# Performance work log

Measured on AMD Instinct MI355X. Metric: run time of the kernel, lower is better.

Reference implementation:

```python
import jax, jax.numpy as jnp
import numpy as np

B, N, C = 4, 2048, 768
H = 12
DH = C // H
HID = int(C * 4.0)
SCALE = DH ** -0.5
EPS = 1e-5


def layernorm(x, g, b):
    mu = jnp.mean(x, axis=-1, keepdims=True)
    var = jnp.var(x, axis=-1, keepdims=True)
    return (x - mu) * jax.lax.rsqrt(var + EPS) * g + b


def setup_inputs() -> dict:
    key = jax.random.key(0)
    ks = jax.random.split(key, 10)
    s = lambda fan_in: 1.0 / np.sqrt(fan_in)
    return {
        "x": jax.random.normal(ks[0], (B, N, C), dtype=jnp.float32),
        "ln1_g": jnp.ones((C,), jnp.float32),
        "ln1_b": jnp.zeros((C,), jnp.float32),
        "w_qkv": jax.random.uniform(ks[1], (C, 3 * C), jnp.float32, -s(C), s(C)),
        "w_proj": jax.random.uniform(ks[2], (C, C), jnp.float32, -s(C), s(C)),
        "b_proj": jnp.zeros((C,), jnp.float32),
        "ln2_g": jnp.ones((C,), jnp.float32),
        "ln2_b": jnp.zeros((C,), jnp.float32),
        "w_fc1": jax.random.uniform(ks[3], (C, HID), jnp.float32, -s(C), s(C)),
        "b_fc1": jnp.zeros((HID,), jnp.float32),
        "w_fc2": jax.random.uniform(ks[4], (HID, C), jnp.float32, -s(HID), s(HID)),
        "b_fc2": jnp.zeros((C,), jnp.float32),
    }


def reference(x, ln1_g, ln1_b, w_qkv, w_proj, b_proj, ln2_g, ln2_b, w_fc1, b_fc1, w_fc2, b_fc2):
    # --- attention branch ---
    h = layernorm(x, ln1_g, ln1_b)                       # [B,N,C]
    qkv = (h @ w_qkv).reshape(B, N, 3, H, DH)
    q = qkv[:, :, 0].transpose(0, 2, 1, 3)               # [B,H,N,DH]
    k = qkv[:, :, 1].transpose(0, 2, 1, 3)
    v = qkv[:, :, 2].transpose(0, 2, 1, 3)
    attn = jnp.einsum('bhnd,bhmd->bhnm', q, k) * SCALE   # [B,H,N,N]
    attn = jax.nn.softmax(attn, axis=-1)
    y = jnp.einsum('bhnm,bhmd->bhnd', attn, v)           # [B,H,N,DH]
    y = y.transpose(0, 2, 1, 3).reshape(B, N, C)
    y = y @ w_proj + b_proj
    x = x + y
    # --- MLP branch ---
    h = layernorm(x, ln2_g, ln2_b)
    h = jax.nn.gelu(h @ w_fc1 + b_fc1, approximate=False)
    h = h @ w_fc2 + b_fc2
    return x + h
```

## Files before the change

kernel.cpp:

```cpp
#include <hip/hip_runtime.h>
#include <stdint.h>

#define DEV __device__ __forceinline__

typedef __attribute__((ext_vector_type(8))) short bf16x8;
typedef __attribute__((ext_vector_type(4))) float f32x4;
typedef __attribute__((ext_vector_type(4))) short s16x4;

DEV short f2bf(float f) {
    union { float f; unsigned u; } v; v.f = f;
    unsigned r = v.u + 0x7fffu + ((v.u >> 16) & 1u);
    return (short)(r >> 16);
}

DEV uint32_t cvtpk(float lo, float hi) {
    uint32_t r;
    asm("v_cvt_pk_bf16_f32 %0, %1, %2" : "=v"(r) : "v"(lo), "v"(hi));
    return r;
}

typedef const unsigned int __attribute__((address_space(1)))* gp1;
typedef unsigned int __attribute__((address_space(3)))* lp3;

DEV void gload16(const void* g, void* l) {
    __builtin_amdgcn_global_load_lds((gp1)g, (lp3)l, 16, 0, 0);
}

DEV void wait4_barrier() { asm volatile("s_waitcnt vmcnt(4)\ns_barrier" ::: "memory"); }
DEV void wait2_barrier() { asm volatile("s_waitcnt vmcnt(2)\ns_barrier" ::: "memory"); }
DEV void wait0_barrier() { asm volatile("s_waitcnt vmcnt(0)\ns_barrier" ::: "memory"); }

__global__ __launch_bounds__(256) void tcvt(
    const float* __restrict__ W, short* __restrict__ WT, int K, int N)
{
    __shared__ float t[32][33];
    int n0 = blockIdx.x * 32, k0 = blockIdx.y * 32;
    int tx = threadIdx.x & 31, ty = threadIdx.x >> 5;
#pragma unroll
    for (int i = 0; i < 32; i += 8)
        t[ty + i][tx] = W[(size_t)(k0 + ty + i) * N + n0 + tx];
    __syncthreads();
#pragma unroll
    for (int i = 0; i < 32; i += 8)
        WT[(size_t)(n0 + ty + i) * K + k0 + tx] = f2bf(t[tx][ty + i]);
}

__global__ __launch_bounds__(256) void ln_bf16(
    const float* __restrict__ x, const float* __restrict__ gam,
    const float* __restrict__ bet, short* __restrict__ out)
{
    const int w = threadIdx.x >> 6, lane = threadIdx.x & 63;
    const size_t row = (size_t)blockIdx.x * 4 + w;
    const float* xr = x + row * 768;
    float4 v[3];
    float s = 0.f, ss = 0.f;
#pragma unroll
    for (int k = 0; k < 3; ++k) {
        v[k] = *(const float4*)(xr + k * 256 + lane * 4);
        s  += v[k].x + v[k].y + v[k].z + v[k].w;
        ss += v[k].x * v[k].x + v[k].y * v[k].y + v[k].z * v[k].z + v[k].w * v[k].w;
    }
#pragma unroll
    for (int i = 1; i < 64; i <<= 1) { s += __shfl_xor(s, i, 64); ss += __shfl_xor(ss, i, 64); }
    const float inv = 1.f / 768.f;
    float mu = s * inv;
    float var = ss * inv - mu * mu;
    float rstd = rsqrtf(var + 1e-5f);
#pragma unroll
    for (int k = 0; k < 3; ++k) {
        int c = k * 256 + lane * 4;
        float vv[4] = { v[k].x, v[k].y, v[k].z, v[k].w };
        s16x4 o;
#pragma unroll
        for (int j = 0; j < 4; ++j)
            o[j] = f2bf((vv[j] - mu) * rstd * gam[c + j] + bet[c + j]);
        *(s16x4*)(out + row * 768 + c) = o;
    }
}

template<int MODE>
DEV void gemm_body(
    const short* __restrict__ A, const short* __restrict__ Bt,
    int M, int N, int K,
    const float* __restrict__ bias, const float* __restrict__ resid,
    float* __restrict__ outf, short* __restrict__ outb,
    short* __restrict__ qo, short* __restrict__ ko, short* __restrict__ vo,
    char* lds)
{
    const int tid = threadIdx.x;
    const int w = tid >> 6, lane = tid & 63;
    const int g = lane >> 4, l15 = lane & 15;
    const int brow = blockIdx.x * 128, bcol = blockIdx.y * 128;
    const int wr = w >> 2, wc = w & 3;
    f32x4 acc[4][2] = {};

    int aoff[4], boff[2];
#pragma unroll
    for (int m = 0; m < 4; ++m) {
        int ra = wr * 64 + m * 16 + l15;
        aoff[m] = ra * 64 + ((g * 16) ^ (((ra >> 1) & 3) << 4));
    }
#pragma unroll
    for (int n = 0; n < 2; ++n) {
        int rb = wc * 32 + n * 16 + l15;
        boff[n] = 8192 + rb * 64 + ((g * 16) ^ (((rb >> 1) & 3) << 4));
    }
    const int dStage = tid * 16;
    const char* pA; const char* pB;
    {
        int r = dStage >> 6, b = dStage & 63;
        int bs = b ^ (((r >> 1) & 3) << 4);
        pA = (const char*)(A  + (size_t)(brow + r) * K) + bs;
        pB = (const char*)(Bt + (size_t)(bcol + r) * K) + bs;
    }

#define GSTAGE(BUF, OFF) do { \
    gload16(pA + (OFF), lds + (BUF) * 16384 + dStage); \
    gload16(pB + (OFF), lds + (BUF) * 16384 + 8192 + dStage); } while (0)

    const int KT = K >> 5;
    GSTAGE(0, 0);
    GSTAGE(1, 64);
    wait2_barrier();

    const int NM = KT / 3;
    for (int mi = 0; mi < NM; ++mi) {
#pragma unroll
        for (int u = 0; u < 3; ++u) {
            const int s = mi * 3 + u;
            if (s + 2 < KT) GSTAGE((u + 2) % 3, (u + 2) * 64);
            bf16x8 af[4], bfg[2];
#pragma unroll
            for (int m = 0; m < 4; ++m)
                af[m]  = *(const bf16x8*)(lds + u * 16384 + aoff[m]);
#pragma unroll
            for (int n = 0; n < 2; ++n)
                bfg[n] = *(const bf16x8*)(lds + u * 16384 + boff[n]);
#pragma unroll
            for (int m = 0; m < 4; ++m)
#pragma unroll
                for (int n = 0; n < 2; ++n)
                    acc[m][n] = __builtin_amdgcn_mfma_f32_16x16x32_bf16(af[m], bfg[n], acc[m][n], 0, 0, 0);
            if (s + 1 < KT) {
                if (s + 2 < KT) wait2_barrier();
                else            wait0_barrier();
            }
        }
        pA += 192; pB += 192;
    }
#undef GSTAGE

#pragma unroll
    for (int m = 0; m < 4; ++m) {
#pragma unroll
        for (int n = 0; n < 2; ++n) {
#pragma unroll
            for (int j = 0; j < 4; ++j) {
                int r = brow + wr * 64 + m * 16 + g * 4 + j;
                int c = bcol + wc * 32 + n * 16 + l15;
                float v = acc[m][n][j];
                if (MODE == 0) {
                    int which = c / 768, cc = c % 768;
                    int h = cc >> 6, d = cc & 63;
                    int b_ = r >> 11, nn = r & 2047;
                    size_t bh = (size_t)b_ * 12 + h;
                    if (which == 0)      qo[(bh * 2048 + nn) * 64 + d] = f2bf(v * 0.18033688011112042f);
                    else if (which == 1) ko[(bh * 2048 + nn) * 64 + d] = f2bf(v);
                    else                 vo[(bh * 64 + d) * 2048 + nn] = f2bf(v);
                } else if (MODE == 1) {
                    outf[(size_t)r * N + c] = v + bias[c] + resid[(size_t)r * N + c];
                } else {
                    float t = v + bias[c];
                    float ge = 0.5f * t * (1.0f + erff(t * 0.70710678118654752f));
                    outb[(size_t)r * N + c] = f2bf(ge);
                }
            }
        }
    }
}

__global__ __launch_bounds__(512, 6) void g_qkv(
    const short* A, const short* Bt, int M, int N, int K,
    short* qo, short* ko, short* vo)
{
    __shared__ __align__(16) char lds[49152];
    gemm_body<0>(A, Bt, M, N, K, nullptr, nullptr, nullptr, nullptr, qo, ko, vo, lds);
}
__global__ __launch_bounds__(512, 6) void g_proj(
    const short* A, const short* Bt, int M, int N, int K,
    const float* bias, const float* resid, float* outf)
{
    __shared__ __align__(16) char lds[49152];
    gemm_body<1>(A, Bt, M, N, K, bias, resid, outf, nullptr, nullptr, nullptr, nullptr, lds);
}
__global__ __launch_bounds__(512, 6) void g_fc1(
    const short* A, const short* Bt, int M, int N, int K,
    const float* bias, short* outb)
{
    __shared__ __align__(16) char lds[49152];
    gemm_body<2>(A, Bt, M, N, K, bias, nullptr, nullptr, outb, nullptr, nullptr, nullptr, lds);
}
__global__ __launch_bounds__(512, 6) void g_fc2(
    const short* A, const short* Bt, int M, int N, int K,
    const float* bias, const float* resid, float* outf)
{
    __shared__ __align__(16) char lds[49152];
    gemm_body<1>(A, Bt, M, N, K, bias, resid, outf, nullptr, nullptr, nullptr, nullptr, lds);
}

__global__ __launch_bounds__(256, 3) void attn_fwd(
    const short* __restrict__ Q, const short* __restrict__ Kg,
    const short* __restrict__ Vt, short* __restrict__ Y)
{
    __shared__ __align__(16) char alds[43008];
    const int tid = threadIdx.x, w = tid >> 6, lane = tid & 63;
    const int g = lane >> 4, l15 = lane & 15;
    const int bid = blockIdx.y * gridDim.x + blockIdx.x;
    const int nwg = gridDim.x * gridDim.y;
    const int logical = (bid & 7) * (nwg >> 3) + (bid >> 3);
    const int bh = logical >> 4;
    const int q0 = (logical & 15) * 128 + w * 32;
    const short* Qb = Q  + (size_t)bh * 2048 * 64;
    const short* Kb = Kg + (size_t)bh * 2048 * 64;
    const short* Vb = Vt + (size_t)bh * 64 * 2048;

    bf16x8 qf[2][2];
#pragma unroll
    for (int m = 0; m < 2; ++m)
#pragma unroll
        for (int kk = 0; kk < 2; ++kk)
            qf[m][kk] = *(const bf16x8*)(Qb + (size_t)(q0 + m * 16 + l15) * 64 + kk * 32 + g * 8);

    f32x4 accO[2][4] = {};
    float lpart[2] = { 0.f, 0.f };

    int koff[2][2], voff[4], poff[2], pwoff[2][2];
#pragma unroll
    for (int n = 0; n < 2; ++n) {
        int key = n * 16 + l15;
#pragma unroll
        for (int kk = 0; kk < 2; ++kk)
            koff[kk][n] = key * 128 + ((kk * 64 + g * 16) ^ ((key & 7) << 4));
    }
#pragma unroll
    for (int n = 0; n < 4; ++n) {
        int d = n * 16 + l15;
        voff[n] = 16384 + d * 64 + ((g * 16) ^ (((d >> 1) & 3) << 4));
    }
#pragma unroll
    for (int m = 0; m < 2; ++m) {
        int qr = m * 16 + l15;
        poff[m] = 32768 + w * 2560 + qr * 80 + g * 16;
#pragma unroll
        for (int n = 0; n < 2; ++n)
            pwoff[m][n] = 32768 + w * 2560 + qr * 80 + n * 32 + g * 8;
    }
    int dK, dV; const char* pK3; const char* pV3;
    {
        int bb = w * 1024;
        int L = bb + lane * 16;
        int rk = L >> 7, bk_ = L & 127;
        int bsk = bk_ ^ ((rk & 7) << 4);
        dK = bb;
        pK3 = (const char*)(Kb + (size_t)rk * 64) + bsk;
        int rv = L >> 6, bv = L & 63;
        int bsv = bv ^ (((rv >> 1) & 3) << 4);
        dV = bb;
        pV3 = (const char*)(Vb + (size_t)rv * 2048) + bsv;
    }
    gload16(pK3,        alds + dK);
    gload16(pV3,        alds + 16384 + dV);
    gload16(pK3 + 4096, alds + dK + 4096);
    gload16(pV3 + 64,   alds + 16384 + dV + 4096);
    gload16(pK3 + 8192, alds + dK + 8192);
    gload16(pV3 + 128,  alds + 16384 + dV + 8192);
    pK3 += 3 * 4096; pV3 += 3 * 64;
    wait4_barrier();

    for (int tm = 0; tm < 16; ++tm) {
#pragma unroll
        for (int tu = 0; tu < 4; ++tu) {
            const int t = tm * 4 + tu;
            if (t + 3 < 64) {
                gload16(pK3, alds + dK + ((tu + 3) & 3) * 4096);
                gload16(pV3, alds + 16384 + dV + ((tu + 3) & 3) * 4096);
                pK3 += 4096; pV3 += 64;
            }

            f32x4 s2[2][2] = {};
            __builtin_amdgcn_s_setprio(1);
#pragma unroll
            for (int kk = 0; kk < 2; ++kk) {
                bf16x8 kf[2];
#pragma unroll
                for (int n = 0; n < 2; ++n)
                    kf[n] = *(const bf16x8*)(alds + tu * 4096 + koff[kk][n]);
#pragma unroll
                for (int m = 0; m < 2; ++m)
#pragma unroll
                    for (int n = 0; n < 2; ++n)
                        s2[m][n] = __builtin_amdgcn_mfma_f32_16x16x32_bf16(kf[n], qf[m][kk], s2[m][n], 0, 0, 0);
            }
            __builtin_amdgcn_s_setprio(0);

#pragma unroll
            for (int m = 0; m < 2; ++m)
#pragma unroll
                for (int n = 0; n < 2; ++n) {
                    float e0 = __builtin_amdgcn_exp2f(s2[m][n][0]);
                    float e1 = __builtin_amdgcn_exp2f(s2[m][n][1]);
                    float e2 = __builtin_amdgcn_exp2f(s2[m][n][2]);
                    float e3 = __builtin_amdgcn_exp2f(s2[m][n][3]);
                    lpart[m] += (e0 + e1) + (e2 + e3);
                    uint2 pk; pk.x = cvtpk(e0, e1); pk.y = cvtpk(e2, e3);
                    *(uint2*)(alds + pwoff[m][n]) = pk;
                }

            __builtin_amdgcn_s_setprio(1);
            {
                bf16x8 vf[4], pf[2];
#pragma unroll
                for (int n = 0; n < 4; ++n)
                    vf[n] = *(const bf16x8*)(alds + tu * 4096 + voff[n]);
#pragma unroll
                for (int m = 0; m < 2; ++m)
                    pf[m] = *(const bf16x8*)(alds + poff[m]);
#pragma unroll
                for (int m = 0; m < 2; ++m)
#pragma unroll
                    for (int n = 0; n < 4; ++n)
                        accO[m][n] = __builtin_amdgcn_mfma_f32_16x16x32_bf16(pf[m], vf[n], accO[m][n], 0, 0, 0);
            }
            __builtin_amdgcn_s_setprio(0);

            if (t < 61)       wait4_barrier();
            else if (t == 61) wait2_barrier();
            else if (t == 62) wait0_barrier();
        }
    }

#pragma unroll
    for (int m = 0; m < 2; ++m) {
        lpart[m] += __shfl_xor(lpart[m], 16, 64);
        lpart[m] += __shfl_xor(lpart[m], 32, 64);
    }

    int b_ = bh / 12, h = bh % 12;
#pragma unroll
    for (int m = 0; m < 2; ++m) {
        float linv[4];
#pragma unroll
        for (int j = 0; j < 4; ++j)
            linv[j] = 1.0f / __shfl(lpart[m], g * 4 + j, 64);
#pragma unroll
        for (int n = 0; n < 4; ++n)
#pragma unroll
            for (int j = 0; j < 4; ++j) {
                int qq = q0 + m * 16 + g * 4 + j;
                int d = n * 16 + l15;
                Y[((size_t)b_ * 2048 + qq) * 768 + h * 64 + d] = f2bf(accO[m][n][j] * linv[j]);
            }
    }
}

extern "C" void kernel_launch(void* const* d_in, const int* in_sizes, int n_in,
                              void* d_out, int out_size, void* d_ws, size_t ws_size,
                              hipStream_t stream)
{
    const float* x      = (const float*)d_in[0];
    const float* ln1_g  = (const float*)d_in[1];
    const float* ln1_b  = (const float*)d_in[2];
    const float* w_qkv  = (const float*)d_in[3];
    const float* w_proj = (const float*)d_in[4];
    const float* b_proj = (const float*)d_in[5];
    const float* ln2_g  = (const float*)d_in[6];
    const float* ln2_b  = (const float*)d_in[7];
    const float* w_fc1  = (const float*)d_in[8];
    const float* b_fc1  = (const float*)d_in[9];
    const float* w_fc2  = (const float*)d_in[10];
    const float* b_fc2  = (const float*)d_in[11];

    char* ws = (char*)d_ws;
    size_t off = 0;
    auto alloc = [&](size_t bytes) -> void* {
        void* p = ws + off; off += (bytes + 255) & ~(size_t)255; return p;
    };
    short* wqkvT = (short*)alloc((size_t)2304 * 768 * 2);
    short* wprojT= (short*)alloc((size_t)768 * 768 * 2);
    short* wfc1T = (short*)alloc((size_t)3072 * 768 * 2);
    short* wfc2T = (short*)alloc((size_t)768 * 3072 * 2);
    short* h1    = (short*)alloc((size_t)8192 * 768 * 2);
    short* qb    = (short*)alloc((size_t)48 * 2048 * 64 * 2);
    short* kb    = (short*)alloc((size_t)48 * 2048 * 64 * 2);
    short* vtb   = (short*)alloc((size_t)48 * 64 * 2048 * 2);
    short* yb    = (short*)alloc((size_t)8192 * 768 * 2);
    float* X1    = (float*)alloc((size_t)8192 * 768 * 4);
    short* h2    = (short*)alloc((size_t)8192 * 768 * 2);
    short* h3    = (short*)alloc((size_t)8192 * 3072 * 2);

    tcvt<<<dim3(2304 / 32, 768 / 32),  256, 0, stream>>>(w_qkv,  wqkvT,  768,  2304);
    tcvt<<<dim3(768 / 32,  768 / 32),  256, 0, stream>>>(w_proj, wprojT, 768,  768);
    tcvt<<<dim3(3072 / 32, 768 / 32),  256, 0, stream>>>(w_fc1,  wfc1T,  768,  3072);
    tcvt<<<dim3(768 / 32,  3072 / 32), 256, 0, stream>>>(w_fc2,  wfc2T,  3072, 768);

    ln_bf16<<<2048, 256, 0, stream>>>(x, ln1_g, ln1_b, h1);

    g_qkv<<<dim3(64, 18), 512, 0, stream>>>(h1, wqkvT, 8192, 2304, 768, qb, kb, vtb);

    attn_fwd<<<dim3(16, 48), 256, 0, stream>>>(qb, kb, vtb, yb);

    g_proj<<<dim3(64, 6), 512, 0, stream>>>(yb, wprojT, 8192, 768, 768, b_proj, x, X1);

    ln_bf16<<<2048, 256, 0, stream>>>(X1, ln2_g, ln2_b, h2);

    g_fc1<<<dim3(64, 24), 512, 0, stream>>>(h2, wfc1T, 8192, 3072, 768, b_fc1, h3);

    g_fc2<<<dim3(64, 6), 512, 0, stream>>>(h3, wfc2T, 8192, 768, 3072, b_fc2, X1, (float*)d_out);
}
```

Baseline: 268.7 us.

## Use 1024-thread GEMM blocks with 16 waves and merge weight conversion kernels

The GEMM kernels now launch 1024 threads, or 16 waves, per 128x128 tile. Each wave computes a 32x32 sub-tile instead of 64x32, and each thread issues one global-to-LDS load per stage instead of two (A or B, chosen by thread id), with the waitcnt adjusted to match. The goal is more latency hiding and fewer accumulator registers per wave, at the cost of more LDS fragment reads per MFMA and heavier barriers across 16 waves. Separately, the four weight transpose/convert launches are merged into one kernel to cut launch overhead.

```diff
diff --git a/kernel.cpp b/kernel.cpp
--- a/kernel.cpp
+++ b/kernel.cpp
@@ -28,13 +28,23 @@
 
 DEV void wait4_barrier() { asm volatile("s_waitcnt vmcnt(4)\ns_barrier" ::: "memory"); }
 DEV void wait2_barrier() { asm volatile("s_waitcnt vmcnt(2)\ns_barrier" ::: "memory"); }
+DEV void wait1_barrier() { asm volatile("s_waitcnt vmcnt(1)\ns_barrier" ::: "memory"); }
 DEV void wait0_barrier() { asm volatile("s_waitcnt vmcnt(0)\ns_barrier" ::: "memory"); }
 
-__global__ __launch_bounds__(256) void tcvt(
-    const float* __restrict__ W, short* __restrict__ WT, int K, int N)
+__global__ __launch_bounds__(256) void tcvt4(
+    const float* __restrict__ W0, short* __restrict__ T0,
+    const float* __restrict__ W1, short* __restrict__ T1,
+    const float* __restrict__ W2, short* __restrict__ T2,
+    const float* __restrict__ W3, short* __restrict__ T3)
 {
     __shared__ float t[32][33];
-    int n0 = blockIdx.x * 32, k0 = blockIdx.y * 32;
+    int bid = blockIdx.x;
+    const float* W; short* WT; int K, N, nx, lb;
+    if (bid < 1728)      { W = W0; WT = T0; K = 768;  N = 2304; nx = 72; lb = bid; }
+    else if (bid < 2304) { W = W1; WT = T1; K = 768;  N = 768;  nx = 24; lb = bid - 1728; }
+    else if (bid < 4608) { W = W2; WT = T2; K = 768;  N = 3072; nx = 96; lb = bid - 2304; }
+    else                 { W = W3; WT = T3; K = 3072; N = 768;  nx = 24; lb = bid - 4608; }
+    int n0 = (lb % nx) * 32, k0 = (lb / nx) * 32;
     int tx = threadIdx.x & 31, ty = threadIdx.x >> 5;
 #pragma unroll
     for (int i = 0; i < 32; i += 8)
@@ -92,12 +102,12 @@
     const int g = lane >> 4, l15 = lane & 15;
     const int brow = blockIdx.x * 128, bcol = blockIdx.y * 128;
     const int wr = w >> 2, wc = w & 3;
-    f32x4 acc[4][2] = {};
-
-    int aoff[4], boff[2];
-#pragma unroll
-    for (int m = 0; m < 4; ++m) {
-        int ra = wr * 64 + m * 16 + l15;
+    f32x4 acc[2][2] = {};
+
+    int aoff[2], boff[2];
+#pragma unroll
+    for (int m = 0; m < 2; ++m) {
+        int ra = wr * 32 + m * 16 + l15;
         aoff[m] = ra * 64 + ((g * 16) ^ (((ra >> 1) & 3) << 4));
     }
 #pragma unroll
@@ -106,22 +116,21 @@
         boff[n] = 8192 + rb * 64 + ((g * 16) ^ (((rb >> 1) & 3) << 4));
     }
     const int dStage = tid * 16;
-    const char* pA; const char* pB;
+    const char* pSrc;
     {
         int r = dStage >> 6, b = dStage & 63;
         int bs = b ^ (((r >> 1) & 3) << 4);
-        pA = (const char*)(A  + (size_t)(brow + r) * K) + bs;
-        pB = (const char*)(Bt + (size_t)(bcol + r) * K) + bs;
-    }
-
-#define GSTAGE(BUF, OFF) do { \
-    gload16(pA + (OFF), lds + (BUF) * 16384 + dStage); \
-    gload16(pB + (OFF), lds + (BUF) * 16384 + 8192 + dStage); } while (0)
+        pSrc = (tid < 512)
+             ? (const char*)(A  + (size_t)(brow + r) * K) + bs
+             : (const char*)(Bt + (size_t)(bcol + (r - 128)) * K) + bs;
+    }
+
+#define GSTAGE(BUF, OFF) gload16(pSrc + (OFF), lds + (BUF) * 16384 + dStage)
 
     const int KT = K >> 5;
     GSTAGE(0, 0);
     GSTAGE(1, 64);
-    wait2_barrier();
+    wait1_barrier();
 
     const int NM = KT / 3;
     for (int mi = 0; mi < NM; ++mi) {
@@ -129,34 +138,34 @@
         for (int u = 0; u < 3; ++u) {
             const int s = mi * 3 + u;
             if (s + 2 < KT) GSTAGE((u + 2) % 3, (u + 2) * 64);
-            bf16x8 af[4], bfg[2];
-#pragma unroll
-            for (int m = 0; m < 4; ++m)
+            bf16x8 af[2], bfg[2];
+#pragma unroll
+            for (int m = 0; m < 2; ++m)
                 af[m]  = *(const bf16x8*)(lds + u * 16384 + aoff[m]);
 #pragma unroll
             for (int n = 0; n < 2; ++n)
                 bfg[n] = *(const bf16x8*)(lds + u * 16384 + boff[n]);
 #pragma unroll
-            for (int m = 0; m < 4; ++m)
+            for (int m = 0; m < 2; ++m)
 #pragma unroll
                 for (int n = 0; n < 2; ++n)
                     acc[m][n] = __builtin_amdgcn_mfma_f32_16x16x32_bf16(af[m], bfg[n], acc[m][n], 0, 0, 0);
             if (s + 1 < KT) {
-                if (s + 2 < KT) wait2_barrier();
+                if (s + 2 < KT) wait1_barrier();
                 else            wait0_barrier();
             }
         }
-        pA += 192; pB += 192;
+        pSrc += 192;
     }
 #undef GSTAGE
 
 #pragma unroll
-    for (int m = 0; m < 4; ++m) {
+    for (int m = 0; m < 2; ++m) {
 #pragma unroll
         for (int n = 0; n < 2; ++n) {
 #pragma unroll
             for (int j = 0; j < 4; ++j) {
-                int r = brow + wr * 64 + m * 16 + g * 4 + j;
+                int r = brow + wr * 32 + m * 16 + g * 4 + j;
                 int c = bcol + wc * 32 + n * 16 + l15;
                 float v = acc[m][n][j];
                 if (MODE == 0) {
@@ -179,28 +188,28 @@
     }
 }
 
-__global__ __launch_bounds__(512, 6) void g_qkv(
+__global__ __launch_bounds__(1024, 8) void g_qkv(
     const short* A, const short* Bt, int M, int N, int K,
     short* qo, short* ko, short* vo)
 {
     __shared__ __align__(16) char lds[49152];
     gemm_body<0>(A, Bt, M, N, K, nullptr, nullptr, nullptr, nullptr, qo, ko, vo, lds);
 }
-__global__ __launch_bounds__(512, 6) void g_proj(
+__global__ __launch_bounds__(1024, 8) void g_proj(
     const short* A, const short* Bt, int M, int N, int K,
     const float* bias, const float* resid, float* outf)
 {
     __shared__ __align__(16) char lds[49152];
     gemm_body<1>(A, Bt, M, N, K, bias, resid, outf, nullptr, nullptr, nullptr, nullptr, lds);
 }
-__global__ __launch_bounds__(512, 6) void g_fc1(
+__global__ __launch_bounds__(1024, 8) void g_fc1(
     const short* A, const short* Bt, int M, int N, int K,
     const float* bias, short* outb)
 {
     __shared__ __align__(16) char lds[49152];
     gemm_body<2>(A, Bt, M, N, K, bias, nullptr, nullptr, outb, nullptr, nullptr, nullptr, lds);
 }
-__global__ __launch_bounds__(512, 6) void g_fc2(
+__global__ __launch_bounds__(1024, 8) void g_fc2(
     const short* A, const short* Bt, int M, int N, int K,
     const float* bias, const float* resid, float* outf)
 {
@@ -398,22 +407,20 @@
     short* h2    = (short*)alloc((size_t)8192 * 768 * 2);
     short* h3    = (short*)alloc((size_t)8192 * 3072 * 2);
 
-    tcvt<<<dim3(2304 / 32, 768 / 32),  256, 0, stream>>>(w_qkv,  wqkvT,  768,  2304);
-    tcvt<<<dim3(768 / 32,  768 / 32),  256, 0, stream>>>(w_proj, wprojT, 768,  768);
-    tcvt<<<dim3(3072 / 32, 768 / 32),  256, 0, stream>>>(w_fc1,  wfc1T,  768,  3072);
-    tcvt<<<dim3(768 / 32,  3072 / 32), 256, 0, stream>>>(w_fc2,  wfc2T,  3072, 768);
+    tcvt4<<<6912, 256, 0, stream>>>(w_qkv, wqkvT, w_proj, wprojT,
+                                    w_fc1, wfc1T, w_fc2, wfc2T);
 
     ln_bf16<<<2048, 256, 0, stream>>>(x, ln1_g, ln1_b, h1);
 
-    g_qkv<<<dim3(64, 18), 512, 0, stream>>>(h1, wqkvT, 8192, 2304, 768, qb, kb, vtb);
+    g_qkv<<<dim3(64, 18), 1024, 0, stream>>>(h1, wqkvT, 8192, 2304, 768, qb, kb, vtb);
 
     attn_fwd<<<dim3(16, 48), 256, 0, stream>>>(qb, kb, vtb, yb);
 
-    g_proj<<<dim3(64, 6), 512, 0, stream>>>(yb, wprojT, 8192, 768, 768, b_proj, x, X1);
+    g_proj<<<dim3(64, 6), 1024, 0, stream>>>(yb, wprojT, 8192, 768, 768, b_proj, x, X1);
 
     ln_bf16<<<2048, 256, 0, stream>>>(X1, ln2_g, ln2_b, h2);
 
-    g_fc1<<<dim3(64, 24), 512, 0, stream>>>(h2, wfc1T, 8192, 3072, 768, b_fc1, h3);
-
-    g_fc2<<<dim3(64, 6), 512, 0, stream>>>(h3, wfc2T, 8192, 768, 3072, b_fc2, X1, (float*)d_out);
-}
+    g_fc1<<<dim3(64, 24), 1024, 0, stream>>>(h2, wfc1T, 8192, 3072, 768, b_fc1, h3);
+
+    g_fc2<<<dim3(64, 6), 1024, 0, stream>>>(h3, wfc2T, 8192, 768, 3072, b_fc2, X1, (float*)d_out);
+}
```

Result: faster. 261.9 us (median of 2 runs) (-2.5%).
